# Kernel tuning notes

Hardware: AMD Instinct MI355X
Metric: run time of the kernel (lower is better)

## Reference

```python
import jax, jax.numpy as jnp
import numpy as np
from jax import lax


def squash(vec):
    # vec: [..., caps, dim]; squash along last dim (dim=2 in original layout [B, caps, dim])
    lensq = jnp.sum(vec * vec, axis=2)
    length = jnp.sqrt(lensq)
    scale = (lensq / (1.0 + lensq) / length)[:, :, None]
    return vec * scale


def setup_inputs() -> dict:
    key = jax.random.key(0)
    ks = jax.random.split(key, 6)
    stdv = 1.0 / np.sqrt(1152.0)
    return {
        "x": jax.random.normal(ks[0], (512, 1, 28, 28), dtype=jnp.float32),
        "conv1_w": jax.random.normal(ks[1], (256, 1, 9, 9), dtype=jnp.float32) * 0.05,
        "conv1_b": jax.random.normal(ks[2], (256,), dtype=jnp.float32) * 0.01,
        "conv2_w": jax.random.normal(ks[3], (256, 256, 9, 9), dtype=jnp.float32) * 0.01,
        "conv2_b": jax.random.normal(ks[4], (256,), dtype=jnp.float32) * 0.01,
        "caps_w": jax.random.uniform(ks[5], (1152, 8, 160), dtype=jnp.float32, minval=-stdv, maxval=stdv),
        "b_prior": jnp.zeros((1152, 10), dtype=jnp.float32),
    }


def reference(x, conv1_w, conv1_b, conv2_w, conv2_b, caps_w, b_prior):
    n_iterations = 3
    output_caps, output_dim = 10, 16
    dn = ("NCHW", "OIHW", "NCHW")

    # conv1 + relu: [N,1,28,28] -> [N,256,20,20]
    h = lax.conv_general_dilated(x, conv1_w, (1, 1), "VALID", dimension_numbers=dn)
    h = jax.nn.relu(h + conv1_b[None, :, None, None])

    # first capsule layer: conv k=9 s=2 -> [N,256,6,6]
    h = lax.conv_general_dilated(h, conv2_w, (2, 2), "VALID", dimension_numbers=dn)
    h = h + conv2_b[None, :, None, None]
    N, C, H, W = h.shape
    # [N, 32, 8, H, W] -> [N, 32, H, W, 8] -> [N, 32*H*W, 8]
    u = h.reshape(N, 32, 8, H, W).transpose(0, 1, 3, 4, 2).reshape(N, 32 * H * W, 8)
    u = squash(u)  # [N, 1152, 8]

    # prediction vectors: u_hat [N, 1152, 10, 16]
    u_hat = jnp.einsum("bid,ido->bio", u, caps_w).reshape(N, 1152, output_caps, output_dim)

    # dynamic routing-by-agreement
    c = jax.nn.softmax(b_prior, axis=1)  # [1152, 10]
    s = jnp.sum(c[None, :, :, None] * u_hat, axis=1)  # [N, 10, 16]
    v = squash(s)
    b_batch = jnp.broadcast_to(b_prior, (N, 1152, output_caps))
    for _ in range(n_iterations):
        b_batch = b_batch + jnp.sum(u_hat * v[:, None, :, :], axis=-1)  # agreement
        c = jax.nn.softmax(b_batch, axis=2)[..., None]  # [N, 1152, 10, 1]
        s = jnp.sum(c * u_hat, axis=1)
        v = squash(s)

    probs = jnp.sqrt(jnp.sum(v * v, axis=2))  # [N, 10]
    return (v, probs)
```

## Files before the change

kernel.cpp:

```cpp
#include <hip/hip_runtime.h>


#define N_IMG 512
#define RG 4

typedef __attribute__((ext_vector_type(8))) short bf16x8;
typedef __attribute__((ext_vector_type(4))) float f32x4;
typedef __attribute__((ext_vector_type(4))) unsigned int u32x4;

__device__ __forceinline__ unsigned short f2bf(float v) {
  unsigned int uu = __float_as_uint(v);
  uu += 0x7FFF + ((uu >> 16) & 1);
  return (unsigned short)(uu >> 16);
}
__device__ __forceinline__ float bf2f(unsigned short h) {
  return __uint_as_float(((unsigned int)h) << 16);
}
__device__ __forceinline__ int swz16(int row) {
  return (row ^ ((row >> 3) & 7)) << 4;
}

__global__ __launch_bounds__(256) void repack_b_kernel(
    const float* __restrict__ w2, unsigned short* __restrict__ bph,
    unsigned short* __restrict__ bpl) {
  __shared__ float slab[82 * 16 * 17];
  const int n = blockIdx.x, c = blockIdx.y;
  const int tid = threadIdx.x;
  for (int e = tid; e < 81 * 256; e += 256) {
    const int row = e / 81;
    const int rs = e - row * 81;
    const int co = row >> 4, ci = row & 15;
    slab[(rs * 16 + co) * 17 + ci] =
        w2[((size_t)(n * 16 + co) * 256 + c * 16 + ci) * 81 + rs];
  }
  __syncthreads();
  const int lane = tid & 63;
  const int l15 = lane & 15;
  const int lh = lane >> 5;
  const int cio8 = ((lane >> 4) & 1) * 8;
  for (int tt = tid >> 6; tt < 41; tt += 4) {
    const int rs = 2 * tt + lh;
    unsigned int hw[4], lw[4];
#pragma unroll
    for (int jp = 0; jp < 4; ++jp) {
      unsigned short h2[2], l2[2];
#pragma unroll
      for (int e = 0; e < 2; ++e) {
        const int j = jp * 2 + e;
        float v = (rs < 81) ? slab[(rs * 16 + l15) * 17 + cio8 + j] : 0.0f;
        unsigned short hh = f2bf(v);
        h2[e] = hh;
        l2[e] = f2bf(v - bf2f(hh));
      }
      hw[jp] = (unsigned int)h2[0] | ((unsigned int)h2[1] << 16);
      lw[jp] = (unsigned int)l2[0] | ((unsigned int)l2[1] << 16);
    }
    const size_t off = (((size_t)n * 656 + c * 41 + tt) * 64 + lane) * 8;
    *(u32x4*)(bph + off) = (u32x4){hw[0], hw[1], hw[2], hw[3]};
    *(u32x4*)(bpl + off) = (u32x4){lw[0], lw[1], lw[2], lw[3]};
  }
}

__global__ __launch_bounds__(160) void repack_cw_kernel(
    const float* __restrict__ cw, float* __restrict__ cwt) {
  __shared__ float t[8][160];
  const int i = blockIdx.x;
  const int od = threadIdx.x;
#pragma unroll
  for (int k = 0; k < 8; ++k) t[k][od] = cw[((size_t)i * 8 + k) * 160 + od];
  __syncthreads();
  float4 o0 = {t[0][od], t[1][od], t[2][od], t[3][od]};
  float4 o1 = {t[4][od], t[5][od], t[6][od], t[7][od]};
  float4* dst = (float4*)(cwt + ((size_t)i * 160 + od) * 8);
  dst[0] = o0;
  dst[1] = o1;
}

__global__ __launch_bounds__(256) void c0_kernel(const float* __restrict__ bp,
                                                 float* __restrict__ c0b) {
  const int i = blockIdx.x * 256 + threadIdx.x;
  if (i >= 1152) return;
  float b[10];
  float m = -1e30f;
#pragma unroll
  for (int o = 0; o < 10; ++o) {
    b[o] = bp[i * 10 + o];
    m = fmaxf(m, b[o]);
  }
  float sum = 0.0f;
#pragma unroll
  for (int o = 0; o < 10; ++o) {
    b[o] = __expf(b[o] - m);
    sum += b[o];
  }
  const float inv = 1.0f / sum;
#pragma unroll
  for (int o = 0; o < 10; ++o) c0b[i * 10 + o] = b[o] * inv;
}

__global__ __launch_bounds__(256) void gemm_s0_kernel(
    const float* __restrict__ u, const float* __restrict__ cw,
    const float* __restrict__ c0b, float* __restrict__ s0p) {
  __shared__ float a_l[64 * 257];
  __shared__ float b_l[64 * 160];
  __shared__ float c0_l[320];
  const int mt = blockIdx.x;
  const int ks = blockIdx.y;
  const int m0 = mt * 64;
  const int tid = threadIdx.x;
  const int mb = tid >> 4;
  const int ob = (tid & 15) * 10;

  for (int i = tid; i < 320; i += 256) c0_l[i] = c0b[(ks * 32) * 10 + i];
  for (int idx = tid; idx < 16384; idx += 256) {
    const int m = idx >> 8, kk = idx & 255;
    a_l[m * 257 + kk] = u[(size_t)(m0 + m) * 9216 + ks * 256 + kk];
  }

  float acc[4][10];
#pragma unroll
  for (int r = 0; r < 4; ++r)
#pragma unroll
    for (int c = 0; c < 10; ++c) acc[r][c] = 0.0f;

#pragma unroll 1
  for (int kc = 0; kc < 4; ++kc) {
    __syncthreads();
    for (int idx = tid; idx < 10240; idx += 256) {
      const int kk = idx / 160, od = idx - kk * 160;
      const int kg = kc * 64 + kk;
      b_l[kk * 160 + od] = cw[((size_t)ks * 256 + kg) * 160 + od] *
                           c0_l[(kg >> 3) * 10 + (od >> 4)];
    }
    __syncthreads();
#pragma unroll 4
    for (int kk = 0; kk < 64; ++kk) {
      float a4[4];
#pragma unroll
      for (int r = 0; r < 4; ++r)
        a4[r] = a_l[(mb * 4 + r) * 257 + kc * 64 + kk];
      const float* bp_ = &b_l[kk * 160 + ob];
#pragma unroll
      for (int c = 0; c < 10; ++c) {
        const float bv = bp_[c];
#pragma unroll
        for (int r = 0; r < 4; ++r) acc[r][c] = fmaf(a4[r], bv, acc[r][c]);
      }
    }
  }

#pragma unroll
  for (int r = 0; r < 4; ++r) {
#pragma unroll
    for (int c = 0; c < 10; ++c) {
      s0p[((size_t)ks * N_IMG + m0 + mb * 4 + r) * 160 + ob + c] = acc[r][c];
    }
  }
}

template <int H>
__device__ __forceinline__ void conv1_half(const float* __restrict__ ib,
                                           const float* __restrict__ w1l,
                                           float* __restrict__ stg, int ch,
                                           int oy, float bv1) {
  float a[10];
#pragma unroll
  for (int ox = 0; ox < 10; ++ox) a[ox] = bv1;
#pragma unroll
  for (int r = 0; r < 9; ++r) {
    float row[20];
    const float4* rp = (const float4*)&ib[(oy + r) * 28 + H * 8];
#pragma unroll
    for (int q = 0; q < 5; ++q) {
      float4 v4 = rp[q];
      row[4 * q + 0] = v4.x; row[4 * q + 1] = v4.y;
      row[4 * q + 2] = v4.z; row[4 * q + 3] = v4.w;
    }
#pragma unroll
    for (int s = 0; s < 9; ++s) {
      const float wval = w1l[ch * 81 + r * 9 + s];
#pragma unroll
      for (int ox = 0; ox < 10; ++ox)
        a[ox] = fmaf(row[ox + s + 2 * H], wval, a[ox]);
    }
  }
  float2* dst = (float2*)&stg[oy * 20 + H * 10];
#pragma unroll
  for (int q = 0; q < 5; ++q) {
    float2 v2;
    v2.x = fmaxf(a[2 * q + 0], 0.0f);
    v2.y = fmaxf(a[2 * q + 1], 0.0f);
    dst[q] = v2;
  }
}

__global__ __launch_bounds__(512, 1) void fused_conv_kernel(
    const float* __restrict__ x, const float* __restrict__ w1,
    const float* __restrict__ b1, const unsigned short* __restrict__ bph,
    const unsigned short* __restrict__ bpl, const float* __restrict__ b2,
    float* __restrict__ u) {
  __shared__ __align__(16) char smem[115008];
  float* stg = (float*)(smem + 51776);
  float* img = (float*)(smem + 103488);
  float* w1l = (float*)(smem + 109760);
  float* b1l = (float*)(smem + 114944);
  float* mrg = (float*)smem;
  float* sq = (float*)smem;

  const int bp2 = blockIdx.x;
  const int tid = threadIdx.x;
  const int wid = tid >> 6;
  const int g = wid & 3;
  const int kpar = wid >> 2;
  const int lane = tid & 63;
  const int l15 = lane & 15;
  const int lq4 = lane >> 4;
  const int lqb = lq4 & 1;
  const int lh = lane >> 5;

  int rowb[5];
  bool okm[5];
#pragma unroll
  for (int mt = 0; mt < 5; ++mt) {
    const int m = mt * 16 + l15;
    okm[mt] = (m < 72);
    const int mm = okm[mt] ? m : 0;
    const int im = (mm >= 36) ? 1 : 0;
    const int p = mm - 36 * im;
    const int oy = p / 6, ox = p - 6 * oy;
    rowb[mt] = im * 400 + 40 * oy + 2 * ox;
  }

  for (int i = tid; i < 1568; i += 512) img[i] = x[bp2 * 1568 + i];
  if (tid < 16) {
    *(int*)(smem + (tid >> 2) * 12944 + 804 * 16 + (tid & 3) * 4) = 0;
  }

  f32x4 acc[5][4];
#pragma unroll
  for (int mt = 0; mt < 5; ++mt)
#pragma unroll
    for (int nn = 0; nn < 4; ++nn) acc[mt][nn] = (f32x4){0.f, 0.f, 0.f, 0.f};

  const char* hbase = smem + lqb * 12944;
  const char* lbase = smem + 25888 + lqb * 12944;
  const int tt0 = kpar ? 21 : 0;
  const int tt1 = kpar ? 41 : 21;
  const int nk = tt1 - tt0;

#define MFMA_STEP(CBH, CBL, J, DOPF)                                       \
  {                                                                        \
    const int rs_ = 2 * (tt0 + (J)) + lh;                                  \
    const int r_ = (rs_ * 57) >> 9;                                        \
    const int s_ = rs_ - 9 * r_;                                           \
    const int rs20_ = 20 * r_ + s_;                                        \
    const bool okrs_ = (rs_ <= 80);                                        \
    bf16x8 ah[5], al[5];                                                   \
    _Pragma("unroll") for (int mt = 0; mt < 5; ++mt) {                     \
      const int row_ = (okm[mt] && okrs_) ? (rowb[mt] + rs20_) : 800;      \
      const int ad_ = swz16(row_);                                         \
      ah[mt] = *(const bf16x8*)(hbase + ad_);                              \
      al[mt] = *(const bf16x8*)(lbase + ad_);                              \
    }                                                                      \
    _Pragma("unroll") for (int mt = 0; mt < 5; ++mt) {                     \
      _Pragma("unroll") for (int nn = 0; nn < 4; ++nn) {                   \
        acc[mt][nn] = __builtin_amdgcn_mfma_f32_16x16x32_bf16(             \
            al[mt], CBH[nn], acc[mt][nn], 0, 0, 0);                        \
        acc[mt][nn] = __builtin_amdgcn_mfma_f32_16x16x32_bf16(             \
            ah[mt], CBL[nn], acc[mt][nn], 0, 0, 0);                        \
        acc[mt][nn] = __builtin_amdgcn_mfma_f32_16x16x32_bf16(             \
            ah[mt], CBH[nn], acc[mt][nn], 0, 0, 0);                        \
      }                                                                    \
    }                                                                      \
    if ((DOPF) && (J) + 2 < nk) {                                          \
      _Pragma("unroll") for (int nn = 0; nn < 4; ++nn) {                   \
        CBH[nn] = *(const bf16x8*)(pb[nn] + (size_t)((J) + 2) * 512);      \
        CBL[nn] = *(const bf16x8*)(pl[nn] + (size_t)((J) + 2) * 512);      \
      }                                                                    \
    }                                                                      \
  }

#pragma unroll 1
  for (int c = 0; c < 16; ++c) {
    const unsigned short* pb[4];
    const unsigned short* pl[4];
#pragma unroll
    for (int nn = 0; nn < 4; ++nn) {
      const size_t base =
          ((size_t)(g * 4 + nn) * 656 + c * 41 + tt0) * 512 + lane * 8;
      pb[nn] = bph + base;
      pl[nn] = bpl + base;
    }
    bf16x8 cbh0[4], cbl0[4], cbh1[4], cbl1[4];
#pragma unroll
    for (int nn = 0; nn < 4; ++nn) {
      cbh0[nn] = *(const bf16x8*)(pb[nn]);
      cbl0[nn] = *(const bf16x8*)(pl[nn]);
      cbh1[nn] = *(const bf16x8*)(pb[nn] + 512);
      cbl1[nn] = *(const bf16x8*)(pl[nn] + 512);
    }

    __syncthreads();
    for (int i = tid; i < 1296; i += 512) w1l[i] = w1[c * 1296 + i];
    if (tid < 16) b1l[tid] = b1[c * 16 + tid];
    __syncthreads();

    for (int t = tid; t < 1280; t += 512) {
      const int half = (t >= 640) ? 1 : 0;
      const int rest = t - half * 640;
      const int ig = rest / 320;
      const int r2 = rest - ig * 320;
      const int ch = r2 & 15;
      const int oy = r2 >> 4;
      const float* ib = &img[ig * 784];
      float* sb = &stg[(ig * 16 + ch) * 404];
      const float bv1 = b1l[ch];
      if (half == 0)
        conv1_half<0>(ib, w1l, sb, ch, oy, bv1);
      else
        conv1_half<1>(ib, w1l, sb, ch, oy, bv1);
    }
    __syncthreads();

    for (int t = tid; t < 800; t += 512) {
      const int ig = t / 400;
      const int pos = t - ig * 400;
      const int ad = swz16(t);
      unsigned int hw[8], lw[8];
#pragma unroll
      for (int jp = 0; jp < 8; ++jp) {
        unsigned short h2[2], l2[2];
#pragma unroll
        for (int e = 0; e < 2; ++e) {
          const float v = stg[(ig * 16 + jp * 2 + e) * 404 + pos];
          const unsigned short hh = f2bf(v);
          h2[e] = hh;
          l2[e] = f2bf(v - bf2f(hh));
        }
        hw[jp] = (unsigned int)h2[0] | ((unsigned int)h2[1] << 16);
        lw[jp] = (unsigned int)l2[0] | ((unsigned int)l2[1] << 16);
      }
      *(u32x4*)(smem + ad) = (u32x4){hw[0], hw[1], hw[2], hw[3]};
      *(u32x4*)(smem + 12944 + ad) = (u32x4){hw[4], hw[5], hw[6], hw[7]};
      *(u32x4*)(smem + 25888 + ad) = (u32x4){lw[0], lw[1], lw[2], lw[3]};
      *(u32x4*)(smem + 38832 + ad) = (u32x4){lw[4], lw[5], lw[6], lw[7]};
    }
    __syncthreads();

    int j = 0;
#pragma unroll 1
    for (; j + 1 < nk; j += 2) {
      MFMA_STEP(cbh0, cbl0, j, 1);
      MFMA_STEP(cbh1, cbl1, j + 1, 1);
    }
    if (j < nk) MFMA_STEP(cbh0, cbl0, j, 0);
  }
#undef MFMA_STEP

  __syncthreads();
  if (kpar == 1) {
#pragma unroll
    for (int mt = 0; mt < 5; ++mt)
#pragma unroll
      for (int nn = 0; nn < 4; ++nn)
        *(f32x4*)(mrg + ((((g * 5 + mt) * 4 + nn) * 64 + lane) << 2)) =
            acc[mt][nn];
  }
  __syncthreads();
  if (kpar == 0) {
#pragma unroll
    for (int mt = 0; mt < 5; ++mt)
#pragma unroll
      for (int nn = 0; nn < 4; ++nn)
        acc[mt][nn] +=
            *(const f32x4*)(mrg + ((((g * 5 + mt) * 4 + nn) * 64 + lane) << 2));
  }
  __syncthreads();
  if (kpar == 0) {
    float b2v[4];
#pragma unroll
    for (int nn = 0; nn < 4; ++nn) b2v[nn] = b2[(g * 4 + nn) * 16 + l15];
#pragma unroll
    for (int mt = 0; mt < 5; ++mt) {
#pragma unroll
      for (int i = 0; i < 4; ++i) {
        const int m = mt * 16 + lq4 * 4 + i;
        if (m < 72) {
          const int im = (m >= 36) ? 1 : 0;
          const int p36 = m - 36 * im;
#pragma unroll
          for (int nn = 0; nn < 4; ++nn) {
            sq[(im * 256 + (g * 4 + nn) * 16 + l15) * 36 + p36] =
                acc[mt][nn][i] + b2v[nn];
          }
        }
      }
    }
  }
  __syncthreads();

  for (int i = tid; i < 2304; i += 512) {
    const int ig = i / 1152;
    const int cap = i - ig * 1152;
    const int gg = cap / 36, yx = cap - 36 * gg;
    float vals[8];
    float lensq = 0.0f;
#pragma unroll
    for (int d = 0; d < 8; ++d) {
      vals[d] = sq[(ig * 256 + gg * 8 + d) * 36 + yx];
      lensq = fmaf(vals[d], vals[d], lensq);
    }
    const float len = sqrtf(lensq);
    const float scale = lensq / (1.0f + lensq) / len;
    float4* dst = (float4*)(u + ((size_t)(bp2 * 2 + ig) * 1152 + cap) * 8);
    float4 lo4, hi4;
    lo4.x = vals[0] * scale; lo4.y = vals[1] * scale;
    lo4.z = vals[2] * scale; lo4.w = vals[3] * scale;
    hi4.x = vals[4] * scale; hi4.y = vals[5] * scale;
    hi4.z = vals[6] * scale; hi4.w = vals[7] * scale;
    dst[0] = lo4; dst[1] = hi4;
  }
}

__global__ __launch_bounds__(256) void routing_a_kernel(
    const float* __restrict__ u, const float* __restrict__ cwt,
    const float* __restrict__ b_prior, const float* __restrict__ vsum,
    float* __restrict__ s_part) {
  __shared__ float u_l[RG * 16 * 8];
  __shared__ float uhat[RG][16][161];
  __shared__ float v_l[RG * 160];
  __shared__ float bp_l[32 * 10];
  __shared__ float c_l[RG * 16 * 10];
  __shared__ float s_acc[RG * 160];

  const int gb = blockIdx.x;
  const int ch = blockIdx.y;
  const int cap0 = ch * 32;
  const int b0 = gb * RG;
  const int tid = threadIdx.x;

  for (int i = tid; i < RG * 160; i += 256) {
    const int g = i / 160, od = i - g * 160;
    v_l[i] = vsum[(b0 + g) * 160 + od];
    s_acc[i] = 0.0f;
  }
  for (int i = tid; i < 320; i += 256) bp_l[i] = b_prior[cap0 * 10 + i];

#pragma unroll 1
  for (int cc = 0; cc < 2; ++cc) {
    const int c16 = cap0 + cc * 16;
    __syncthreads();
    for (int i = tid; i < RG * 128; i += 256) {
      const int g = i >> 7, off = i & 127;
      u_l[g * 128 + off] = u[((size_t)(b0 + g) * 1152 + c16) * 8 + off];
    }
    __syncthreads();

    for (int e = tid; e < 2560; e += 256) {
      const int i = e / 160, od = e - i * 160;
      const float4* wp =
          (const float4*)(cwt + ((size_t)(c16 + i) * 160 + od) * 8);
      const float4 wa = wp[0], wb = wp[1];
#pragma unroll
      for (int g = 0; g < RG; ++g) {
        const float* up = &u_l[(g * 16 + i) * 8];
        float a = up[0] * wa.x;
        a = fmaf(up[1], wa.y, a);
        a = fmaf(up[2], wa.z, a);
        a = fmaf(up[3], wa.w, a);
        a = fmaf(up[4], wb.x, a);
        a = fmaf(up[5], wb.y, a);
        a = fmaf(up[6], wb.z, a);
        a = fmaf(up[7], wb.w, a);
        uhat[g][i][od] = a;
      }
    }
    __syncthreads();

    for (int e = tid; e < RG * 160; e += 256) {
      const int g = e / 160;
      const int r = e - g * 160;
      const int i = r / 10, o = r - i * 10;
      float agg = 0.0f;
#pragma unroll
      for (int d = 0; d < 16; ++d)
        agg = fmaf(uhat[g][i][o * 16 + d], v_l[g * 160 + o * 16 + d], agg);
      c_l[e] = bp_l[(cc * 16 + i) * 10 + o] + agg;
    }
    __syncthreads();

    if (tid < RG * 16) {
      const int g = tid >> 4, i = tid & 15;
      float bb[10];
      float m = -1e30f;
#pragma unroll
      for (int o = 0; o < 10; ++o) {
        bb[o] = c_l[(g * 16 + i) * 10 + o];
        m = fmaxf(m, bb[o]);
      }
      float sum = 0.0f;
#pragma unroll
      for (int o = 0; o < 10; ++o) {
        bb[o] = __expf(bb[o] - m);
        sum += bb[o];
      }
      const float inv = 1.0f / sum;
#pragma unroll
      for (int o = 0; o < 10; ++o) c_l[(g * 16 + i) * 10 + o] = bb[o] * inv;
    }
    __syncthreads();

    for (int e = tid; e < RG * 160; e += 256) {
      const int g = e / 160, od = e - g * 160;
      const int o = od >> 4;
      float a = 0.0f;
#pragma unroll
      for (int i = 0; i < 16; ++i)
        a = fmaf(c_l[(g * 16 + i) * 10 + o], uhat[g][i][od], a);
      s_acc[e] += a;
    }
  }
  __syncthreads();

  for (int e = tid; e < RG * 160; e += 256) {
    const int g = e / 160, od = e - g * 160;
    s_part[((size_t)ch * N_IMG + b0 + g) * 160 + od] = s_acc[e];
  }
}

__global__ __launch_bounds__(192) void routing_b_kernel(
    const float* __restrict__ s_part, int nchunk, float* __restrict__ v_out,
    float* __restrict__ probs, float* __restrict__ vsum, int mode) {
  __shared__ float s_l[160];
  __shared__ float scale_l[10];
  __shared__ float len_l[10];
  const int b = blockIdx.x;
  const int t = threadIdx.x;
  if (t < 160) {
    float a = 0.0f;
    for (int ch = 0; ch < nchunk; ++ch)
      a += s_part[((size_t)ch * N_IMG + b) * 160 + t];
    s_l[t] = a;
  }
  __syncthreads();
  if (t < 10) {
    float lensq = 0.0f;
#pragma unroll
    for (int d = 0; d < 16; ++d) {
      const float xv = s_l[t * 16 + d];
      lensq = fmaf(xv, xv, lensq);
    }
    const float len = sqrtf(lensq);
    scale_l[t] = lensq / (1.0f + lensq) / len;
    len_l[t] = lensq / (1.0f + lensq);
  }
  __syncthreads();
  if (t < 160) {
    const float vv = s_l[t] * scale_l[t / 16];
    v_out[b * 160 + t] = vv;
    if (mode == 0) vsum[b * 160 + t] = vv;
    else if (mode == 1) vsum[b * 160 + t] += vv;
  }
  if (t < 10) probs[b * 10 + t] = len_l[t];
}

extern "C" void kernel_launch(void* const* d_in, const int* in_sizes, int n_in,
                              void* d_out, int out_size, void* d_ws,
                              size_t ws_size, hipStream_t stream) {
  const float* x  = (const float*)d_in[0];
  const float* w1 = (const float*)d_in[1];
  const float* b1 = (const float*)d_in[2];
  const float* w2 = (const float*)d_in[3];
  const float* b2 = (const float*)d_in[4];
  const float* cw = (const float*)d_in[5];
  const float* bp = (const float*)d_in[6];

  float* out = (float*)d_out;
  float* v_out = out;
  float* probs = out + N_IMG * 160;

  float* base = (float*)d_ws;
  unsigned short* bph = (unsigned short*)d_ws;
  unsigned short* bpl = bph + (size_t)16 * 656 * 512;
  float* u    = base + 5373952;
  float* vsum = u + 4718592;
  float* c0b  = vsum + 81920;
  float* cwt = base;
  float* sp  = base + 1474560;

  repack_b_kernel<<<dim3(16, 16), 256, 0, stream>>>(w2, bph, bpl);
  fused_conv_kernel<<<256, 512, 0, stream>>>(x, w1, b1, bph, bpl, b2, u);
  c0_kernel<<<5, 256, 0, stream>>>(bp, c0b);
  repack_cw_kernel<<<1152, 160, 0, stream>>>(cw, cwt);
  gemm_s0_kernel<<<dim3(8, 36), 256, 0, stream>>>(u, cw, c0b, sp);
  routing_b_kernel<<<N_IMG, 192, 0, stream>>>(sp, 36, v_out, probs, vsum, 0);
  for (int pass = 1; pass < 4; ++pass) {
    const int mode = (pass < 3) ? 1 : 2;
    routing_a_kernel<<<dim3(N_IMG / RG, 36), 256, 0, stream>>>(u, cwt, bp,
                                                               vsum, sp);
    routing_b_kernel<<<N_IMG, 192, 0, stream>>>(sp, 36, v_out, probs, vsum,
                                                mode);
  }
}
```

Measured before the change: 1.017 ms.

## Warp-specialize conv1 producer and MFMA consumer with double-buffered LDS

Splits the block into producer waves (4-7) that compute conv1, split into bf16 hi/lo and write it straight into a double-buffered swizzled LDS layout, and consumer waves (0-3) that run the MFMA conv2 over the whole K range for the previous chunk. This removes the fp32 staging buffer, the separate conversion pass and the cross-wave K-split reduction, and lets conv1 overlap the MFMA work. The cost is that only half the waves now issue MFMAs, so the matrix pipe may be under-used if conv1 is the shorter stage, and LDS use grows.

```diff
diff --git a/kernel.cpp b/kernel.cpp
--- a/kernel.cpp
+++ b/kernel.cpp
@@ -3,6 +3,13 @@
 
 #define N_IMG 512
 #define RG 4
+
+#define ARRS 12944
+#define BUFS (4 * ARRS)
+#define IMG_OFF (2 * BUFS)
+#define W1L_OFF (IMG_OFF + 6272)
+#define B1L_OFF (W1L_OFF + 10368)
+#define SMEM_SZ (B1L_OFF + 128)
 
 typedef __attribute__((ext_vector_type(8))) short bf16x8;
 typedef __attribute__((ext_vector_type(4))) float f32x4;
@@ -161,8 +168,8 @@
 template <int H>
 __device__ __forceinline__ void conv1_half(const float* __restrict__ ib,
                                            const float* __restrict__ w1l,
-                                           float* __restrict__ stg, int ch,
-                                           int oy, float bv1) {
+                                           char* __restrict__ abase, int ch,
+                                           int oy, int ig, float bv1) {
   float a[10];
 #pragma unroll
   for (int ox = 0; ox < 10; ++ox) a[ox] = bv1;
@@ -184,13 +191,17 @@
         a[ox] = fmaf(row[ox + s + 2 * H], wval, a[ox]);
     }
   }
-  float2* dst = (float2*)&stg[oy * 20 + H * 10];
-#pragma unroll
-  for (int q = 0; q < 5; ++q) {
-    float2 v2;
-    v2.x = fmaxf(a[2 * q + 0], 0.0f);
-    v2.y = fmaxf(a[2 * q + 1], 0.0f);
-    dst[q] = v2;
+  const int arrA = (ch >> 3) * ARRS;
+  const int colB = (ch & 7) * 2;
+  const int rowBase = ig * 400 + oy * 20 + H * 10;
+#pragma unroll
+  for (int q = 0; q < 10; ++q) {
+    const float v = fmaxf(a[q], 0.0f);
+    const unsigned short hi = f2bf(v);
+    const unsigned short lo = f2bf(v - bf2f(hi));
+    const int sb = swz16(rowBase + q);
+    *(unsigned short*)(abase + arrA + sb + colB) = hi;
+    *(unsigned short*)(abase + 2 * ARRS + arrA + sb + colB) = lo;
   }
 }
 
@@ -199,24 +210,19 @@
     const float* __restrict__ b1, const unsigned short* __restrict__ bph,
     const unsigned short* __restrict__ bpl, const float* __restrict__ b2,
     float* __restrict__ u) {
-  __shared__ __align__(16) char smem[115008];
-  float* stg = (float*)(smem + 51776);
-  float* img = (float*)(smem + 103488);
-  float* w1l = (float*)(smem + 109760);
-  float* b1l = (float*)(smem + 114944);
-  float* mrg = (float*)smem;
+  __shared__ __align__(16) char smem[SMEM_SZ];
+  float* img = (float*)(smem + IMG_OFF);
   float* sq = (float*)smem;
 
   const int bp2 = blockIdx.x;
   const int tid = threadIdx.x;
   const int wid = tid >> 6;
-  const int g = wid & 3;
-  const int kpar = wid >> 2;
   const int lane = tid & 63;
   const int l15 = lane & 15;
   const int lq4 = lane >> 4;
   const int lqb = lq4 & 1;
   const int lh = lane >> 5;
+  const int g = wid & 3;
 
   int rowb[5];
   bool okm[5];
@@ -232,25 +238,22 @@
   }
 
   for (int i = tid; i < 1568; i += 512) img[i] = x[bp2 * 1568 + i];
-  if (tid < 16) {
-    *(int*)(smem + (tid >> 2) * 12944 + 804 * 16 + (tid & 3) * 4) = 0;
-  }
+  if (tid < 32) {
+    *(int*)(smem + (tid >> 2) * ARRS + 804 * 16 + (tid & 3) * 4) = 0;
+  }
+  for (int i = tid; i < 1296; i += 512) ((float*)(smem + W1L_OFF))[i] = w1[i];
+  if (tid < 16) ((float*)(smem + B1L_OFF))[tid] = b1[tid];
+  __syncthreads();
 
   f32x4 acc[5][4];
 #pragma unroll
   for (int mt = 0; mt < 5; ++mt)
 #pragma unroll
     for (int nn = 0; nn < 4; ++nn) acc[mt][nn] = (f32x4){0.f, 0.f, 0.f, 0.f};
-
-  const char* hbase = smem + lqb * 12944;
-  const char* lbase = smem + 25888 + lqb * 12944;
-  const int tt0 = kpar ? 21 : 0;
-  const int tt1 = kpar ? 41 : 21;
-  const int nk = tt1 - tt0;
 
 #define MFMA_STEP(CBH, CBL, J, DOPF)                                       \
   {                                                                        \
-    const int rs_ = 2 * (tt0 + (J)) + lh;                                  \
+    const int rs_ = 2 * (J) + lh;                                          \
     const int r_ = (rs_ * 57) >> 9;                                        \
     const int s_ = rs_ - 9 * r_;                                           \
     const int rs20_ = 20 * r_ + s_;                                        \
@@ -272,7 +275,7 @@
             ah[mt], CBH[nn], acc[mt][nn], 0, 0, 0);                        \
       }                                                                    \
     }                                                                      \
-    if ((DOPF) && (J) + 2 < nk) {                                          \
+    if ((DOPF) && (J) + 2 < 41) {                                          \
       _Pragma("unroll") for (int nn = 0; nn < 4; ++nn) {                   \
         CBH[nn] = *(const bf16x8*)(pb[nn] + (size_t)((J) + 2) * 512);      \
         CBL[nn] = *(const bf16x8*)(pl[nn] + (size_t)((J) + 2) * 512);      \
@@ -281,102 +284,71 @@
   }
 
 #pragma unroll 1
-  for (int c = 0; c < 16; ++c) {
-    const unsigned short* pb[4];
-    const unsigned short* pl[4];
-#pragma unroll
-    for (int nn = 0; nn < 4; ++nn) {
-      const size_t base =
-          ((size_t)(g * 4 + nn) * 656 + c * 41 + tt0) * 512 + lane * 8;
-      pb[nn] = bph + base;
-      pl[nn] = bpl + base;
-    }
-    bf16x8 cbh0[4], cbl0[4], cbh1[4], cbl1[4];
-#pragma unroll
-    for (int nn = 0; nn < 4; ++nn) {
-      cbh0[nn] = *(const bf16x8*)(pb[nn]);
-      cbl0[nn] = *(const bf16x8*)(pl[nn]);
-      cbh1[nn] = *(const bf16x8*)(pb[nn] + 512);
-      cbl1[nn] = *(const bf16x8*)(pl[nn] + 512);
-    }
-
-    __syncthreads();
-    for (int i = tid; i < 1296; i += 512) w1l[i] = w1[c * 1296 + i];
-    if (tid < 16) b1l[tid] = b1[c * 16 + tid];
-    __syncthreads();
-
-    for (int t = tid; t < 1280; t += 512) {
-      const int half = (t >= 640) ? 1 : 0;
-      const int rest = t - half * 640;
-      const int ig = rest / 320;
-      const int r2 = rest - ig * 320;
-      const int ch = r2 & 15;
-      const int oy = r2 >> 4;
-      const float* ib = &img[ig * 784];
-      float* sb = &stg[(ig * 16 + ch) * 404];
-      const float bv1 = b1l[ch];
-      if (half == 0)
-        conv1_half<0>(ib, w1l, sb, ch, oy, bv1);
-      else
-        conv1_half<1>(ib, w1l, sb, ch, oy, bv1);
-    }
-    __syncthreads();
-
-    for (int t = tid; t < 800; t += 512) {
-      const int ig = t / 400;
-      const int pos = t - ig * 400;
-      const int ad = swz16(t);
-      unsigned int hw[8], lw[8];
-#pragma unroll
-      for (int jp = 0; jp < 8; ++jp) {
-        unsigned short h2[2], l2[2];
-#pragma unroll
-        for (int e = 0; e < 2; ++e) {
-          const float v = stg[(ig * 16 + jp * 2 + e) * 404 + pos];
-          const unsigned short hh = f2bf(v);
-          h2[e] = hh;
-          l2[e] = f2bf(v - bf2f(hh));
+  for (int it = 0; it <= 16; ++it) {
+    if (wid >= 4) {
+      if (it < 16) {
+        const float* w1l = (float*)(smem + W1L_OFF) + (it & 1) * 1296;
+        const float* b1l = (float*)(smem + B1L_OFF) + (it & 1) * 16;
+        char* abase = smem + (it & 1) * BUFS;
+        for (int t = tid - 256; t < 1280; t += 256) {
+          const int half = (t >= 640) ? 1 : 0;
+          const int rest = t - half * 640;
+          const int ig = rest / 320;
+          const int r2 = rest - ig * 320;
+          const int ch = r2 & 15;
+          const int oy = r2 >> 4;
+          const float* ib = &img[ig * 784];
+          const float bv1 = b1l[ch];
+          if (half == 0)
+            conv1_half<0>(ib, w1l, abase, ch, oy, ig, bv1);
+          else
+            conv1_half<1>(ib, w1l, abase, ch, oy, ig, bv1);
         }
-        hw[jp] = (unsigned int)h2[0] | ((unsigned int)h2[1] << 16);
-        lw[jp] = (unsigned int)l2[0] | ((unsigned int)l2[1] << 16);
-      }
-      *(u32x4*)(smem + ad) = (u32x4){hw[0], hw[1], hw[2], hw[3]};
-      *(u32x4*)(smem + 12944 + ad) = (u32x4){hw[4], hw[5], hw[6], hw[7]};
-      *(u32x4*)(smem + 25888 + ad) = (u32x4){lw[0], lw[1], lw[2], lw[3]};
-      *(u32x4*)(smem + 38832 + ad) = (u32x4){lw[4], lw[5], lw[6], lw[7]};
-    }
-    __syncthreads();
-
-    int j = 0;
+        if (it + 1 < 16) {
+          float* w1n = (float*)(smem + W1L_OFF) + ((it + 1) & 1) * 1296;
+          for (int i = tid - 256; i < 1296; i += 256)
+            w1n[i] = w1[(it + 1) * 1296 + i];
+          if (tid - 256 < 16)
+            ((float*)(smem + B1L_OFF))[((it + 1) & 1) * 16 + (tid - 256)] =
+                b1[(it + 1) * 16 + (tid - 256)];
+        }
+      }
+    } else {
+      if (it >= 1) {
+        const int cc = it - 1;
+        const unsigned short* pb[4];
+        const unsigned short* pl[4];
+#pragma unroll
+        for (int nn = 0; nn < 4; ++nn) {
+          const size_t base =
+              ((size_t)(g * 4 + nn) * 656 + cc * 41) * 512 + lane * 8;
+          pb[nn] = bph + base;
+          pl[nn] = bpl + base;
+        }
+        bf16x8 cbh0[4], cbl0[4], cbh1[4], cbl1[4];
+#pragma unroll
+        for (int nn = 0; nn < 4; ++nn) {
+          cbh0[nn] = *(const bf16x8*)(pb[nn]);
+          cbl0[nn] = *(const bf16x8*)(pl[nn]);
+          cbh1[nn] = *(const bf16x8*)(pb[nn] + 512);
+          cbl1[nn] = *(const bf16x8*)(pl[nn] + 512);
+        }
+        const char* hbase = smem + (cc & 1) * BUFS + lqb * ARRS;
+        const char* lbase = smem + (cc & 1) * BUFS + 2 * ARRS + lqb * ARRS;
+        int j = 0;
 #pragma unroll 1
-    for (; j + 1 < nk; j += 2) {
-      MFMA_STEP(cbh0, cbl0, j, 1);
-      MFMA_STEP(cbh1, cbl1, j + 1, 1);
-    }
-    if (j < nk) MFMA_STEP(cbh0, cbl0, j, 0);
+        for (; j + 1 < 41; j += 2) {
+          MFMA_STEP(cbh0, cbl0, j, 1);
+          MFMA_STEP(cbh1, cbl1, j + 1, 1);
+        }
+        MFMA_STEP(cbh0, cbl0, 40, 0);
+      }
+    }
+    __syncthreads();
   }
 #undef MFMA_STEP
 
-  __syncthreads();
-  if (kpar == 1) {
-#pragma unroll
-    for (int mt = 0; mt < 5; ++mt)
-#pragma unroll
-      for (int nn = 0; nn < 4; ++nn)
-        *(f32x4*)(mrg + ((((g * 5 + mt) * 4 + nn) * 64 + lane) << 2)) =
-            acc[mt][nn];
-  }
-  __syncthreads();
-  if (kpar == 0) {
-#pragma unroll
-    for (int mt = 0; mt < 5; ++mt)
-#pragma unroll
-      for (int nn = 0; nn < 4; ++nn)
-        acc[mt][nn] +=
-            *(const f32x4*)(mrg + ((((g * 5 + mt) * 4 + nn) * 64 + lane) << 2));
-  }
-  __syncthreads();
-  if (kpar == 0) {
+  if (wid < 4) {
     float b2v[4];
 #pragma unroll
     for (int nn = 0; nn < 4; ++nn) b2v[nn] = b2[(g * 4 + nn) * 16 + l15];
```

New measurement: 1.158 ms. 1.14x slower.
